# Kernel tuning notes

Hardware: AMD Instinct MI355X
Metric: run time of the kernel (lower is better)

Reference implementation:

```python
import jax, jax.numpy as jnp
import numpy as np

B, S, D = 2, 2048, 1024
H, HD = 16, 64
FF = 4096
LOCAL_W, RAND_P = 256, 0.2
EPS = 1e-5
NEG = -9e15


def _linear_params(key, din, dout):
    kw, kb = jax.random.split(key)
    bound = 1.0 / np.sqrt(din)
    W = jax.random.uniform(kw, (din, dout), jnp.float32, -bound, bound)
    b = jax.random.uniform(kb, (dout,), jnp.float32, -bound, bound)
    return W, b


def setup_inputs() -> dict:
    key = jax.random.key(0)
    ks = jax.random.split(key, 10)
    x = jax.random.normal(ks[0], (B, S, D), jnp.float32)
    # local + random mask, as in create_local_mask
    i = np.arange(S)[:, None]
    j = np.arange(S)[None, :]
    local = (np.abs(i - j) <= LOCAL_W // 2)
    rnd = np.asarray(jax.random.bernoulli(ks[1], RAND_P, (S, S)))
    mask = jnp.asarray(np.logical_or(local, rnd).astype(np.int32))
    Wq, bq = _linear_params(ks[2], D, D)
    Wk, bk = _linear_params(ks[3], D, D)
    Wv, bv = _linear_params(ks[4], D, D)
    Wo, bo = _linear_params(ks[5], D, D)
    W1, b1 = _linear_params(ks[6], D, FF)
    W2, b2 = _linear_params(ks[7], FF, D)
    g1 = jnp.ones((D,), jnp.float32); be1 = jnp.zeros((D,), jnp.float32)
    g2 = jnp.ones((D,), jnp.float32); be2 = jnp.zeros((D,), jnp.float32)
    return dict(x=x, mask=mask, Wq=Wq, bq=bq, Wk=Wk, bk=bk, Wv=Wv, bv=bv,
                Wo=Wo, bo=bo, W1=W1, b1=b1, W2=W2, b2=b2,
                g1=g1, be1=be1, g2=g2, be2=be2)


def _layernorm(x, g, b):
    mu = jnp.mean(x, axis=-1, keepdims=True)
    var = jnp.mean(jnp.square(x - mu), axis=-1, keepdims=True)
    return (x - mu) * jax.lax.rsqrt(var + EPS) * g + b


def reference(x, mask, Wq, bq, Wk, bk, Wv, bv, Wo, bo, W1, b1, W2, b2, g1, be1, g2, be2):
    scale = jnp.float32(np.sqrt(HD))  # sqrt(head_dim), requires_grad=False
    q = x @ Wq + bq
    k = x @ Wk + bk
    v = x @ Wv + bv
    # faithful to original: view(B, heads, S, head_dim) WITHOUT transpose
    q = q.reshape(B, H, S, HD)
    k = k.reshape(B, H, S, HD)
    v = v.reshape(B, H, S, HD)
    scores = jnp.einsum('bhsd,bhtd->bhst', q / scale, k)  # [B,H,S,S]
    scores = jnp.where(mask == 0, jnp.float32(NEG), scores)
    probs = jax.nn.softmax(scores, axis=-1)
    av = jnp.einsum('bhst,bhtd->bhsd', probs, v)
    # faithful reshape back: view(B, S, head_dim*heads)
    attn_out = av.reshape(B, S, H * HD) @ Wo + bo
    x = _layernorm(x + attn_out, g1, be1)
    ffn = jax.nn.gelu(x @ W1 + b1, approximate=False) @ W2 + b2
    x = _layernorm(x + ffn, g2, be2)
    return x
```

## Files before the change

kernel.cpp:

```cpp
#include <hip/hip_runtime.h>
#include <cstdint>
#include <cstddef>

namespace {

constexpr int kS  = 2048;
constexpr int kD  = 1024;
constexpr int kHD = 64;
constexpr int kTOK = 4096;

typedef float f32x4 __attribute__((ext_vector_type(4)));
typedef __bf16 bf16x8 __attribute__((ext_vector_type(8)));
typedef unsigned short u16x8 __attribute__((ext_vector_type(8)));

__device__ __forceinline__ unsigned short f2b(float f){
  unsigned int u = __builtin_bit_cast(unsigned int, f);
  u += 0x7fffu + ((u >> 16) & 1u);
  return (unsigned short)(u >> 16);
}

__device__ __forceinline__ float b2f(unsigned short u){
  return __builtin_bit_cast(float, (unsigned)u << 16);
}

__device__ __forceinline__ bf16x8 ldfrag(const unsigned short* p){
  return __builtin_bit_cast(bf16x8, *(const u16x8*)p);
}

__device__ __forceinline__ float fexp2(float x){
#if __has_builtin(__builtin_amdgcn_exp2f)
  return __builtin_amdgcn_exp2f(x);
#else
  return exp2f(x);
#endif
}

__device__ __forceinline__ void gl_lds16(const void* g, void* l){
  __builtin_amdgcn_global_load_lds(
      (__attribute__((address_space(1))) void*)(void*)g,
      (__attribute__((address_space(3))) void*)l, 16, 0, 0);
}

__device__ __forceinline__ bf16x8 ld_swz(const unsigned short* tile, int row, int slot){
  return ldfrag(tile + row * 64 + (((slot ^ row) & 7) << 3));
}

__device__ __forceinline__ void stageKt(const unsigned short* Kg, unsigned short* lds,
                                        int wave, int lane, int t0){
  #pragma unroll
  for (int i = 0; i < 2; ++i){
    const int lin = i * 4096 + wave * 1024 + lane * 16;
    const int r = lin >> 7;
    const int sl = (lin >> 4) & 7;
    const int sabs = t0 + r;
    gl_lds16(Kg + (size_t)(sabs >> 4) * 3072 + (sabs & 15) * 64 + (((sl ^ r) & 7) << 3),
             (char*)lds + i * 4096 + wave * 1024);
  }
}

__device__ __forceinline__ void stageVt(const unsigned short* Vh, unsigned short* lds,
                                        int wave, int lane, int t0){
  #pragma unroll
  for (int i = 0; i < 2; ++i){
    const int lin = i * 4096 + wave * 1024 + lane * 16;
    const int r = lin >> 7;
    const int sl = (lin >> 4) & 7;
    gl_lds16(Vh + (size_t)r * kS + t0 + (((sl ^ r) & 7) << 3),
             (char*)lds + i * 4096 + wave * 1024);
  }
}

__global__ __launch_bounds__(256) void cvt_bf16_kern(const float* __restrict__ X,
                                                     unsigned short* __restrict__ Y){
  int i = blockIdx.x * 256 + threadIdx.x;
  float4 v = ((const float4*)X)[i];
  ((ushort4*)Y)[i] = make_ushort4(f2b(v.x), f2b(v.y), f2b(v.z), f2b(v.w));
}

__global__ __launch_bounds__(256) void maskbits_kern(const int* __restrict__ mask,
                                                     unsigned long long* __restrict__ mb){
  const int gw   = (blockIdx.x * 256 + threadIdx.x) >> 6;
  const int lane = threadIdx.x & 63;
  const int row  = gw >> 5, word = gw & 31;
  const int key  = ((lane >> 2) & 3) * 16 + ((lane >> 4) & 3) * 4 + (lane & 3);
  const int m = mask[(size_t)row * kS + word * 64 + key];
  const unsigned long long b = __ballot(m != 0);
  if (lane == 0) mb[(size_t)row * 32 + word] = b;
}

__global__ __launch_bounds__(256) void catbias_kern(const float* __restrict__ a,
                                                    const float* __restrict__ b,
                                                    const float* __restrict__ c,
                                                    float* __restrict__ o){
  int i = blockIdx.x * 256 + threadIdx.x;
  float v = (i < 1024) ? a[i] : ((i < 2048) ? b[i - 1024] : c[i - 2048]);
  o[i] = v;
}

__global__ __launch_bounds__(256) void wtrans_kern(const float* __restrict__ W,
                                                   unsigned short* __restrict__ Wt,
                                                   int K, int N){
  __shared__ float t[32][33];
  int n0 = blockIdx.x * 32, k0 = blockIdx.y * 32;
  int tx = threadIdx.x & 31, ty = threadIdx.x >> 5;
  #pragma unroll
  for (int i = 0; i < 32; i += 8)
    t[ty + i][tx] = W[(size_t)(k0 + ty + i) * N + n0 + tx];
  __syncthreads();
  #pragma unroll
  for (int i = 0; i < 32; i += 8)
    Wt[(size_t)(n0 + ty + i) * K + k0 + tx] = f2b(t[tx][ty + i]);
}

__global__ __launch_bounds__(256) void vtrans_kern(const unsigned short* __restrict__ QKV,
                                                   unsigned short* __restrict__ Vt){
  __shared__ unsigned short t[64][65];
  int bh = blockIdx.y, s0 = blockIdx.x * 64;
  const int rowbase = (bh >> 4) * 2048 + (bh & 15) * 128;
  const unsigned short* Vg = QKV + (size_t)rowbase * 3072 + 2048;
  unsigned short* Vth = Vt + (size_t)bh * kHD * kS;
  int tx = threadIdx.x & 63, ty = threadIdx.x >> 6;
  #pragma unroll
  for (int i = 0; i < 64; i += 4){
    const int s = s0 + ty + i;
    t[ty + i][tx] = Vg[(size_t)(s >> 4) * 3072 + (s & 15) * 64 + tx];
  }
  __syncthreads();
  #pragma unroll
  for (int i = 0; i < 64; i += 4)
    Vth[(size_t)(ty + i) * kS + s0 + tx] = t[tx][ty + i];
}

template <int ACT_GELU, int SPLITK, int SCLQ>
__global__ __launch_bounds__(512, 2) void gemm256_kern(const unsigned short* __restrict__ A,
                                                       const unsigned short* __restrict__ Bt,
                                                       const float* __restrict__ bias,
                                                       unsigned short* __restrict__ C,
                                                       int M, int N, int K){
  __shared__ unsigned short As[2][2][128 * 64];
  __shared__ unsigned short Bs[2][2][128 * 64];
  int bid = blockIdx.y * gridDim.x + blockIdx.x;
  const int nwg = gridDim.x * gridDim.y;
  bid = (bid & 7) * (nwg >> 3) + (bid >> 3);
  const int bx = bid % gridDim.x, by = bid / gridDim.x;
  const int m0 = by << 8, n0 = bx << 8;
  const int tid  = threadIdx.x;
  const int wave = tid >> 6, lane = tid & 63;
  const int wr = wave >> 2, wc = wave & 3;
  const int lr = lane & 15, lk = lane >> 4;
  const int kz   = K / SPLITK;
  const int kbeg = (SPLITK > 1) ? blockIdx.z * kz : 0;
  const int NT   = kz >> 6;
  const int srow = tid >> 3;
  const int scol = ((tid & 7) ^ (srow & 7)) << 3;
  const unsigned short* Ag = A  + (size_t)(m0 + srow) * K + kbeg + scol;
  const unsigned short* Bg = Bt + (size_t)(n0 + srow) * K + kbeg + scol;
  const int dst = tid * 8;
  const int sk0 = ((    lk) ^ (lr & 7)) << 3;
  const int sk1 = ((4 + lk) ^ (lr & 7)) << 3;
  const int aro = lr * 64;
  const int bro = ((wc & 1) * 64 + lr) * 64;
  const int bh_ = wc >> 1;

  f32x4 acc[8][4] = {};
  bf16x8 aR[4][2], bR[2][2][2];

  auto stA = [&](int b, int h, int kt){
    const unsigned short* s = Ag + (size_t)(h * 128) * K + kt * 64;
    gl_lds16(s,                  &As[b][h][dst]);
    gl_lds16(s + (size_t)64 * K, &As[b][h][4096 + dst]);
  };
  auto stB = [&](int b, int h, int kt){
    const unsigned short* s = Bg + (size_t)(h * 128) * K + kt * 64;
    gl_lds16(s,                  &Bs[b][h][dst]);
    gl_lds16(s + (size_t)64 * K, &Bs[b][h][4096 + dst]);
  };

#define LOAD_A(b, MH) { \
  _Pragma("unroll") for (int mp = 0; mp < 4; ++mp){ \
    aR[mp][0] = ldfrag(&As[b][wr][aro + ((MH) * 64 + mp * 16) * 64 + sk0]); \
    aR[mp][1] = ldfrag(&As[b][wr][aro + ((MH) * 64 + mp * 16) * 64 + sk1]); } }
#define LOAD_B(b, NH) { \
  _Pragma("unroll") for (int np = 0; np < 2; ++np){ \
    bR[NH][np][0] = ldfrag(&Bs[b][bh_][bro + ((NH) * 32 + np * 16) * 64 + sk0]); \
    bR[NH][np][1] = ldfrag(&Bs[b][bh_][bro + ((NH) * 32 + np * 16) * 64 + sk1]); } }
#define QMFMA(MH, NH) { \
  _Pragma("unroll") for (int kk = 0; kk < 2; ++kk) \
  _Pragma("unroll") for (int mp = 0; mp < 4; ++mp) \
  _Pragma("unroll") for (int np = 0; np < 2; ++np) \
    acc[(MH)*4+mp][(NH)*2+np] = __builtin_amdgcn_mfma_f32_16x16x32_bf16( \
        aR[mp][kk], bR[NH][np][kk], acc[(MH)*4+mp][(NH)*2+np], 0, 0, 0); }
#define PHASE_TAIL(QM) \
  asm volatile("s_barrier" ::: "memory"); \
  asm volatile("s_waitcnt lgkmcnt(0)" ::: "memory"); \
  __builtin_amdgcn_sched_barrier(0); \
  __builtin_amdgcn_s_setprio(1); \
  QM; \
  __builtin_amdgcn_s_setprio(0); \
  __builtin_amdgcn_sched_barrier(0); \
  asm volatile("s_barrier" ::: "memory");

  stA(0, 0, 0); stB(0, 0, 0); stB(0, 1, 0); stA(0, 1, 0);
  asm volatile("s_waitcnt vmcnt(4)" ::: "memory");
  asm volatile("s_barrier" ::: "memory");

  for (int t = 0; t < NT; ++t){
    const int b = t & 1, bn = b ^ 1;
    const bool pf = (t + 1 < NT);
    LOAD_A(b, 0); LOAD_B(b, 0);
    if (pf){ stA(bn, 0, t + 1); asm volatile("s_waitcnt vmcnt(4)" ::: "memory"); }
    else   {                    asm volatile("s_waitcnt vmcnt(2)" ::: "memory"); }
    PHASE_TAIL(QMFMA(0, 0));
    LOAD_B(b, 1);
    if (pf){ stB(bn, 0, t + 1); asm volatile("s_waitcnt vmcnt(4)" ::: "memory"); }
    else   {                    asm volatile("s_waitcnt vmcnt(0)" ::: "memory"); }
    PHASE_TAIL(QMFMA(0, 1));
    LOAD_A(b, 1);
    if (pf){ stB(bn, 1, t + 1); }
    PHASE_TAIL(QMFMA(1, 0));
    if (pf){ stA(bn, 1, t + 1); asm volatile("s_waitcnt vmcnt(4)" ::: "memory"); }
    PHASE_TAIL(QMFMA(1, 1));
  }
#undef LOAD_A
#undef LOAD_B
#undef QMFMA
#undef PHASE_TAIL

  unsigned short* Cb = C + (SPLITK > 1 ? (size_t)blockIdx.z * M * N : 0);
  float bvv[4], csc[4];
  #pragma unroll
  for (int n = 0; n < 4; ++n){
    const int col = n0 + wc * 64 + n * 16 + lr;
    bvv[n] = (SPLITK == 1) ? bias[col] : 0.0f;
    csc[n] = (SCLQ && col < 1024) ? 0.18033688011112042f : 1.0f;
  }
  #pragma unroll
  for (int m = 0; m < 8; ++m){
    #pragma unroll
    for (int j = 0; j < 4; ++j){
      const int row = m0 + wr * 128 + m * 16 + lk * 4 + j;
      unsigned short* crow = Cb + (size_t)row * N + n0 + wc * 64 + lr;
      #pragma unroll
      for (int n = 0; n < 4; ++n){
        float v = acc[m][n][j] + bvv[n];
        if (ACT_GELU) v = 0.5f * v * (1.0f + erff(v * 0.70710678118654752f));
        if (SCLQ) v *= csc[n];
        crow[n * 16] = f2b(v);
      }
    }
  }
}

__global__ __launch_bounds__(256) void attn_kern(const unsigned short* __restrict__ QKV,
                                                 const unsigned short* __restrict__ Vt,
                                                 const unsigned long long* __restrict__ mbits,
                                                 unsigned short* __restrict__ O){
  __shared__ unsigned short Ks[2][64 * 64];
  __shared__ unsigned short Vs[2][64 * 64];
  __shared__ unsigned short Ps[4][16 * 64];
  const int tid = threadIdx.x;
  const int wave = tid >> 6, lane = tid & 63;
  const int lr = lane & 15, lk = lane >> 4;
  int bid = blockIdx.y * gridDim.x + blockIdx.x;
  bid = (bid & 7) * 128 + (bid >> 3);
  const int qblk = bid & 31, bh = bid >> 5;
  const int rowbase = (bh >> 4) * 2048 + (bh & 15) * 128;
  const unsigned short* Qg = QKV + (size_t)rowbase * 3072;
  const unsigned short* Kg = Qg + 1024;
  const unsigned short* Vh = Vt + (size_t)bh * kHD * kS;
  const int qbase = qblk * 64 + wave * 16;

  bf16x8 qf[2];
  { const int qr = qbase + lr;
    const unsigned short* qp = Qg + (size_t)(qr >> 4) * 3072 + (qr & 15) * 64 + lk * 8;
    qf[0] = ldfrag(qp); qf[1] = ldfrag(qp + 32); }

  f32x4 accO[4] = {};
  float lsum = 0.f;
  unsigned short* Pw = Ps[wave];
  char* Pwb = (char*)Pw + lr * 128 + ((lk & 1) << 3);
  const int lr7 = lr & 7;

  const unsigned long long* mrp = mbits + (size_t)(qbase + lr) * 32;
  unsigned long long mb = mrp[0];

  stageKt(Kg, Ks[0], wave, lane, 0);
  stageVt(Vh, Vs[0], wave, lane, 0);
  __syncthreads();

  int cur = 0;
  for (int t = 0; t < kS / 64; ++t){
    unsigned long long mbn = 0;
    if (t < kS / 64 - 1){
      stageKt(Kg, Ks[cur ^ 1], wave, lane, (t + 1) * 64);
      stageVt(Vh, Vs[cur ^ 1], wave, lane, (t + 1) * 64);
      mbn = mrp[t + 1];
    }
    f32x4 sa[4] = {};
    #pragma unroll
    for (int kk = 0; kk < 2; ++kk)
      #pragma unroll
      for (int n = 0; n < 4; ++n){
        bf16x8 kf = ld_swz(Ks[cur], n * 16 + lr, kk * 4 + lk);
        sa[n] = __builtin_amdgcn_mfma_f32_16x16x32_bf16(kf, qf[kk], sa[n], 0, 0, 0);
      }
    const unsigned wb = (unsigned)(mb >> (lk * 16));
    float s = 0.f;
    #pragma unroll
    for (int n = 0; n < 4; ++n){
      float p0, p1, p2, p3;
      {
        float v0 = fexp2(sa[n][0]), v1 = fexp2(sa[n][1]);
        float v2 = fexp2(sa[n][2]), v3 = fexp2(sa[n][3]);
        const int s0 = ((int)(wb << (31 - (n * 4 + 0)))) >> 31;
        const int s1 = ((int)(wb << (31 - (n * 4 + 1)))) >> 31;
        const int s2 = ((int)(wb << (31 - (n * 4 + 2)))) >> 31;
        const int s3 = ((int)(wb << (31 - (n * 4 + 3)))) >> 31;
        p0 = __builtin_bit_cast(float, __builtin_bit_cast(int, v0) & s0);
        p1 = __builtin_bit_cast(float, __builtin_bit_cast(int, v1) & s1);
        p2 = __builtin_bit_cast(float, __builtin_bit_cast(int, v2) & s2);
        p3 = __builtin_bit_cast(float, __builtin_bit_cast(int, v3) & s3);
      }
      s += (p0 + p1) + (p2 + p3);
      unsigned r0, r1;
      asm("v_cvt_pk_bf16_f32 %0, %1, %2" : "=v"(r0) : "v"(p0), "v"(p1));
      asm("v_cvt_pk_bf16_f32 %0, %1, %2" : "=v"(r1) : "v"(p2), "v"(p3));
      *(uint2*)(Pwb + (((2 * n + (lk >> 1)) ^ lr7) << 4)) = make_uint2(r0, r1);
    }
    s += __shfl_xor(s, 16);
    s += __shfl_xor(s, 32);
    lsum += s;
    #pragma unroll
    for (int kk = 0; kk < 2; ++kk){
      bf16x8 pf = ld_swz(Pw, lr, kk * 4 + lk);
      #pragma unroll
      for (int dd = 0; dd < 4; ++dd){
        bf16x8 vfr = ld_swz(Vs[cur], dd * 16 + lr, kk * 4 + lk);
        accO[dd] = __builtin_amdgcn_mfma_f32_16x16x32_bf16(pf, vfr, accO[dd], 0, 0, 0);
      }
    }
    mb = mbn;
    __syncthreads();
    cur ^= 1;
  }
  const size_t hoff = (size_t)bh * kS * kHD;
  #pragma unroll
  for (int j = 0; j < 4; ++j){
    const float inv = 1.0f / __shfl(lsum, lk * 4 + j);
    const int row = qbase + lk * 4 + j;
    #pragma unroll
    for (int dd = 0; dd < 4; ++dd)
      O[hoff + (size_t)row * 64 + dd * 16 + lr] = f2b(accO[dd][j] * inv);
  }
}

template <int NP, int PBF16, int OUT_B>
__global__ __launch_bounds__(256) void add_ln_kern(const float* __restrict__ X,
                                                   const void* __restrict__ P,
                                                   const float* __restrict__ bias,
                                                   const float* __restrict__ g,
                                                   const float* __restrict__ be,
                                                   float* __restrict__ Yf,
                                                   unsigned short* __restrict__ Yb){
  const int row = blockIdx.x;
  const int tid = threadIdx.x;
  const size_t pstride = (size_t)kTOK * kD;
  const int idx = row * 256 + tid;
  float r0 = 0.f, r1 = 0.f, r2 = 0.f, r3 = 0.f;
  #pragma unroll
  for (int z = 0; z < NP; ++z){
    if (PBF16){
      ushort4 u = ((const ushort4*)P)[z * (pstride / 4) + idx];
      r0 += b2f(u.x); r1 += b2f(u.y); r2 += b2f(u.z); r3 += b2f(u.w);
    } else {
      float4 p = ((const float4*)P)[z * (pstride / 4) + idx];
      r0 += p.x; r1 += p.y; r2 += p.z; r3 += p.w;
    }
  }
  const float4 bb = ((const float4*)bias)[tid];
  const float4 xv = ((const float4*)X)[idx];
  const float a0 = xv.x + r0 + bb.x, a1 = xv.y + r1 + bb.y;
  const float a2 = xv.z + r2 + bb.z, a3 = xv.w + r3 + bb.w;
  float s = a0 + a1 + a2 + a3;
  float q = a0*a0 + a1*a1 + a2*a2 + a3*a3;
  #pragma unroll
  for (int d = 1; d < 64; d <<= 1){ s += __shfl_xor(s, d); q += __shfl_xor(q, d); }
  __shared__ float red[8];
  const int wave = tid >> 6, lane = tid & 63;
  if (lane == 0){ red[wave] = s; red[4 + wave] = q; }
  __syncthreads();
  s = red[0] + red[1] + red[2] + red[3];
  q = red[4] + red[5] + red[6] + red[7];
  const float mu   = s * (1.0f / kD);
  const float var  = q * (1.0f / kD) - mu * mu;
  const float rstd = rsqrtf(var + 1e-5f);
  const float4 gv = ((const float4*)g)[tid];
  const float4 bv = ((const float4*)be)[tid];
  const float y0 = (a0 - mu) * rstd * gv.x + bv.x;
  const float y1 = (a1 - mu) * rstd * gv.y + bv.y;
  const float y2 = (a2 - mu) * rstd * gv.z + bv.z;
  const float y3 = (a3 - mu) * rstd * gv.w + bv.w;
  ((float4*)Yf)[idx] = make_float4(y0, y1, y2, y3);
  if (OUT_B)
    ((ushort4*)Yb)[idx] = make_ushort4(f2b(y0), f2b(y1), f2b(y2), f2b(y3));
}

}

extern "C" void kernel_launch(void* const* d_in, const int* in_sizes, int n_in,
                              void* d_out, int out_size, void* d_ws, size_t ws_size,
                              hipStream_t stream){
  (void)in_sizes; (void)n_in; (void)out_size;
  const float* x   = (const float*)d_in[0];
  const int*   mask= (const int*)d_in[1];
  const float* Wq  = (const float*)d_in[2];  const float* bq  = (const float*)d_in[3];
  const float* Wk  = (const float*)d_in[4];  const float* bk  = (const float*)d_in[5];
  const float* Wv  = (const float*)d_in[6];  const float* bv  = (const float*)d_in[7];
  const float* Wo  = (const float*)d_in[8];  const float* bo  = (const float*)d_in[9];
  const float* W1  = (const float*)d_in[10]; const float* b1  = (const float*)d_in[11];
  const float* W2  = (const float*)d_in[12]; const float* b2  = (const float*)d_in[13];
  const float* g1  = (const float*)d_in[14]; const float* be1 = (const float*)d_in[15];
  const float* g2  = (const float*)d_in[16]; const float* be2 = (const float*)d_in[17];

  char* ws = (char*)d_ws;
  const size_t MB = 1024 * 1024;
  if (ws_size < 96 * MB) return;

  unsigned short* W2T   = (unsigned short*)(ws + 0 * MB);
  unsigned short* W1T   = (unsigned short*)(ws + 8 * MB);
  unsigned short* WqkvT = (unsigned short*)(ws + 16 * MB);
  unsigned short* WoT   = (unsigned short*)(ws + 22 * MB);
  unsigned short* xb    = (unsigned short*)(ws + 24 * MB);
  unsigned short* qkv   = (unsigned short*)(ws + 32 * MB);
  unsigned short* vt    = (unsigned short*)(ws + 56 * MB);
  unsigned short* av    = (unsigned short*)(ws + 64 * MB);
  unsigned long long* mbits = (unsigned long long*)(ws + 72 * MB);
  float* bqkv           = (float*)(ws + 80 * MB);
  unsigned short* woP   = (unsigned short*)(ws + 32 * MB);
  float* y32            = (float*)(ws + 72 * MB);
  unsigned short* yb    = (unsigned short*)(ws + 88 * MB);
  unsigned short* hb    = (unsigned short*)(ws + 40 * MB);
  unsigned short* w2p   = (unsigned short*)(ws + 8 * MB);

  dim3 blk(256), gblk(512);
  wtrans_kern<<<dim3(32, 32),  blk, 0, stream>>>(Wq, WqkvT,                   1024, 1024);
  wtrans_kern<<<dim3(32, 32),  blk, 0, stream>>>(Wk, WqkvT + 1024 * 1024,     1024, 1024);
  wtrans_kern<<<dim3(32, 32),  blk, 0, stream>>>(Wv, WqkvT + 2 * 1024 * 1024, 1024, 1024);
  wtrans_kern<<<dim3(32, 32),  blk, 0, stream>>>(Wo, WoT, 1024, 1024);
  wtrans_kern<<<dim3(128, 32), blk, 0, stream>>>(W1, W1T, 1024, 4096);
  wtrans_kern<<<dim3(32, 128), blk, 0, stream>>>(W2, W2T, 4096, 1024);
  cvt_bf16_kern<<<dim3(kTOK * kD / 1024), blk, 0, stream>>>(x, xb);
  maskbits_kern<<<dim3(kS * 32 / 4), blk, 0, stream>>>(mask, mbits);
  catbias_kern<<<dim3(12), blk, 0, stream>>>(bq, bk, bv, bqkv);

  gemm256_kern<0,1,1><<<dim3(12, 16), gblk, 0, stream>>>(xb, WqkvT, bqkv, qkv, 4096, 3072, 1024);

  vtrans_kern<<<dim3(32, 32), blk, 0, stream>>>(qkv, vt);
  attn_kern<<<dim3(32, 32), blk, 0, stream>>>(qkv, vt, mbits, av);

  gemm256_kern<0,4,0><<<dim3(4, 16, 4), gblk, 0, stream>>>(av, WoT, bo, woP, 4096, 1024, 1024);
  add_ln_kern<4,1,1><<<dim3(4096), blk, 0, stream>>>(x, woP, bo, g1, be1, y32, yb);

  gemm256_kern<1,1,0><<<dim3(16, 16), gblk, 0, stream>>>(yb, W1T, b1, hb, 4096, 4096, 1024);
  gemm256_kern<0,4,0><<<dim3(4, 16, 4), gblk, 0, stream>>>(hb, W2T, b2, w2p, 4096, 1024, 4096);
  add_ln_kern<4,1,0><<<dim3(4096), blk, 0, stream>>>(y32, w2p, b2, g2, be2, (float*)d_out, nullptr);
}
```

Measured before the change: 268.4 us.

## Merge prep launches, widen attention blocks to 128 queries, use fast erf

The six weight-transpose launches become one kernel, and the bf16 convert, mask-bit and bias-concat launches become another, which cuts launch overhead. The attention kernel now runs 512 threads covering 128 queries per block, so each staged K/V tile is shared by twice as many query rows and global K/V traffic drops, at the cost of more waves waiting on each barrier. GELU now uses an Abramowitz-Stegun polynomial approximation of erf with a hardware reciprocal instead of erff, which costs less arithmetic but loses some accuracy.

```diff
diff --git a/kernel.cpp b/kernel.cpp
--- a/kernel.cpp
+++ b/kernel.cpp
@@ -35,6 +35,19 @@
 #endif
 }
 
+__device__ __forceinline__ float fast_erf(float x){
+  const float ax = fabsf(x);
+#if __has_builtin(__builtin_amdgcn_rcpf)
+  const float t = __builtin_amdgcn_rcpf(1.0f + 0.3275911f * ax);
+#else
+  const float t = 1.0f / (1.0f + 0.3275911f * ax);
+#endif
+  const float y = t * (0.254829592f + t * (-0.284496736f + t * (1.421413741f +
+                  t * (-1.453152027f + t * 1.061405429f))));
+  const float e = fexp2(-ax * ax * 1.4426950408889634f);
+  return copysignf(1.0f - y * e, x);
+}
+
 __device__ __forceinline__ void gl_lds16(const void* g, void* l){
   __builtin_amdgcn_global_load_lds(
       (__attribute__((address_space(1))) void*)(void*)g,
@@ -45,64 +58,70 @@
   return ldfrag(tile + row * 64 + (((slot ^ row) & 7) << 3));
 }
 
-__device__ __forceinline__ void stageKt(const unsigned short* Kg, unsigned short* lds,
-                                        int wave, int lane, int t0){
-  #pragma unroll
-  for (int i = 0; i < 2; ++i){
-    const int lin = i * 4096 + wave * 1024 + lane * 16;
-    const int r = lin >> 7;
-    const int sl = (lin >> 4) & 7;
-    const int sabs = t0 + r;
-    gl_lds16(Kg + (size_t)(sabs >> 4) * 3072 + (sabs & 15) * 64 + (((sl ^ r) & 7) << 3),
-             (char*)lds + i * 4096 + wave * 1024);
-  }
-}
-
-__device__ __forceinline__ void stageVt(const unsigned short* Vh, unsigned short* lds,
-                                        int wave, int lane, int t0){
-  #pragma unroll
-  for (int i = 0; i < 2; ++i){
-    const int lin = i * 4096 + wave * 1024 + lane * 16;
-    const int r = lin >> 7;
-    const int sl = (lin >> 4) & 7;
-    gl_lds16(Vh + (size_t)r * kS + t0 + (((sl ^ r) & 7) << 3),
-             (char*)lds + i * 4096 + wave * 1024);
-  }
-}
-
-__global__ __launch_bounds__(256) void cvt_bf16_kern(const float* __restrict__ X,
-                                                     unsigned short* __restrict__ Y){
-  int i = blockIdx.x * 256 + threadIdx.x;
-  float4 v = ((const float4*)X)[i];
-  ((ushort4*)Y)[i] = make_ushort4(f2b(v.x), f2b(v.y), f2b(v.z), f2b(v.w));
-}
-
-__global__ __launch_bounds__(256) void maskbits_kern(const int* __restrict__ mask,
-                                                     unsigned long long* __restrict__ mb){
-  const int gw   = (blockIdx.x * 256 + threadIdx.x) >> 6;
-  const int lane = threadIdx.x & 63;
-  const int row  = gw >> 5, word = gw & 31;
-  const int key  = ((lane >> 2) & 3) * 16 + ((lane >> 4) & 3) * 4 + (lane & 3);
-  const int m = mask[(size_t)row * kS + word * 64 + key];
-  const unsigned long long b = __ballot(m != 0);
-  if (lane == 0) mb[(size_t)row * 32 + word] = b;
-}
-
-__global__ __launch_bounds__(256) void catbias_kern(const float* __restrict__ a,
-                                                    const float* __restrict__ b,
-                                                    const float* __restrict__ c,
-                                                    float* __restrict__ o){
-  int i = blockIdx.x * 256 + threadIdx.x;
-  float v = (i < 1024) ? a[i] : ((i < 2048) ? b[i - 1024] : c[i - 2048]);
-  o[i] = v;
-}
-
-__global__ __launch_bounds__(256) void wtrans_kern(const float* __restrict__ W,
-                                                   unsigned short* __restrict__ Wt,
-                                                   int K, int N){
+__device__ __forceinline__ void stageK8(const unsigned short* Kg, unsigned short* lds,
+                                        int tid, int t0){
+  const int r = tid >> 3, sl = tid & 7;
+  const int sabs = t0 + r;
+  gl_lds16(Kg + (size_t)(sabs >> 4) * 3072 + (sabs & 15) * 64 + (((sl ^ r) & 7) << 3),
+           (char*)lds + tid * 16);
+}
+
+__device__ __forceinline__ void stageV8(const unsigned short* Vh, unsigned short* lds,
+                                        int tid, int t0){
+  const int r = tid >> 3, sl = tid & 7;
+  gl_lds16(Vh + (size_t)r * kS + t0 + (((sl ^ r) & 7) << 3),
+           (char*)lds + tid * 16);
+}
+
+__global__ __launch_bounds__(256) void prep_misc_kern(const float* __restrict__ x,
+                                                      unsigned short* __restrict__ xb,
+                                                      const int* __restrict__ mask,
+                                                      unsigned long long* __restrict__ mb,
+                                                      const float* __restrict__ bq,
+                                                      const float* __restrict__ bk,
+                                                      const float* __restrict__ bv,
+                                                      float* __restrict__ bqkv){
+  const int b = blockIdx.x;
+  if (b < 4096){
+    const int i = b * 256 + threadIdx.x;
+    float4 v = ((const float4*)x)[i];
+    ((ushort4*)xb)[i] = make_ushort4(f2b(v.x), f2b(v.y), f2b(v.z), f2b(v.w));
+  } else if (b < 20480){
+    const int gw   = ((b - 4096) * 256 + threadIdx.x) >> 6;
+    const int lane = threadIdx.x & 63;
+    const int row  = gw >> 5, word = gw & 31;
+    const int key  = ((lane >> 2) & 3) * 16 + ((lane >> 4) & 3) * 4 + (lane & 3);
+    const int m = mask[(size_t)row * kS + word * 64 + key];
+    const unsigned long long bl = __ballot(m != 0);
+    if (lane == 0) mb[(size_t)row * 32 + word] = bl;
+  } else {
+    const int i = (b - 20480) * 256 + threadIdx.x;
+    float v = (i < 1024) ? bq[i] : ((i < 2048) ? bk[i - 1024] : bv[i - 2048]);
+    bqkv[i] = v;
+  }
+}
+
+__global__ __launch_bounds__(256) void wtrans_all_kern(const float* __restrict__ Wq,
+                                                       const float* __restrict__ Wk,
+                                                       const float* __restrict__ Wv,
+                                                       const float* __restrict__ Wo,
+                                                       const float* __restrict__ W1,
+                                                       const float* __restrict__ W2,
+                                                       unsigned short* __restrict__ WqkvT,
+                                                       unsigned short* __restrict__ WoT,
+                                                       unsigned short* __restrict__ W1T,
+                                                       unsigned short* __restrict__ W2T){
+  const int b = blockIdx.x;
+  const float* W; unsigned short* Wt; int K, N, nx, lb;
+  if      (b < 1024){ W = Wq; Wt = WqkvT;                 K = 1024; N = 1024; nx = 32;  lb = b; }
+  else if (b < 2048){ W = Wk; Wt = WqkvT + 1024 * 1024;   K = 1024; N = 1024; nx = 32;  lb = b - 1024; }
+  else if (b < 3072){ W = Wv; Wt = WqkvT + 2048 * 1024;   K = 1024; N = 1024; nx = 32;  lb = b - 2048; }
+  else if (b < 4096){ W = Wo; Wt = WoT;                   K = 1024; N = 1024; nx = 32;  lb = b - 3072; }
+  else if (b < 8192){ W = W1; Wt = W1T;                   K = 1024; N = 4096; nx = 128; lb = b - 4096; }
+  else              { W = W2; Wt = W2T;                   K = 4096; N = 1024; nx = 32;  lb = b - 8192; }
   __shared__ float t[32][33];
-  int n0 = blockIdx.x * 32, k0 = blockIdx.y * 32;
-  int tx = threadIdx.x & 31, ty = threadIdx.x >> 5;
+  const int n0 = (lb % nx) * 32, k0 = (lb / nx) * 32;
+  const int tx = threadIdx.x & 31, ty = threadIdx.x >> 5;
   #pragma unroll
   for (int i = 0; i < 32; i += 8)
     t[ty + i][tx] = W[(size_t)(k0 + ty + i) * N + n0 + tx];
@@ -243,7 +262,7 @@
       #pragma unroll
       for (int n = 0; n < 4; ++n){
         float v = acc[m][n][j] + bvv[n];
-        if (ACT_GELU) v = 0.5f * v * (1.0f + erff(v * 0.70710678118654752f));
+        if (ACT_GELU) v = 0.5f * v * (1.0f + fast_erf(v * 0.70710678118654752f));
         if (SCLQ) v *= csc[n];
         crow[n * 16] = f2b(v);
       }
@@ -251,24 +270,24 @@
   }
 }
 
-__global__ __launch_bounds__(256) void attn_kern(const unsigned short* __restrict__ QKV,
+__global__ __launch_bounds__(512) void attn_kern(const unsigned short* __restrict__ QKV,
                                                  const unsigned short* __restrict__ Vt,
                                                  const unsigned long long* __restrict__ mbits,
                                                  unsigned short* __restrict__ O){
   __shared__ unsigned short Ks[2][64 * 64];
   __shared__ unsigned short Vs[2][64 * 64];
-  __shared__ unsigned short Ps[4][16 * 64];
+  __shared__ unsigned short Ps[8][16 * 64];
   const int tid = threadIdx.x;
   const int wave = tid >> 6, lane = tid & 63;
   const int lr = lane & 15, lk = lane >> 4;
   int bid = blockIdx.y * gridDim.x + blockIdx.x;
-  bid = (bid & 7) * 128 + (bid >> 3);
-  const int qblk = bid & 31, bh = bid >> 5;
+  bid = (bid & 7) * 64 + (bid >> 3);
+  const int qblk = bid & 15, bh = bid >> 4;
   const int rowbase = (bh >> 4) * 2048 + (bh & 15) * 128;
   const unsigned short* Qg = QKV + (size_t)rowbase * 3072;
   const unsigned short* Kg = Qg + 1024;
   const unsigned short* Vh = Vt + (size_t)bh * kHD * kS;
-  const int qbase = qblk * 64 + wave * 16;
+  const int qbase = qblk * 128 + wave * 16;
 
   bf16x8 qf[2];
   { const int qr = qbase + lr;
@@ -284,16 +303,16 @@
   const unsigned long long* mrp = mbits + (size_t)(qbase + lr) * 32;
   unsigned long long mb = mrp[0];
 
-  stageKt(Kg, Ks[0], wave, lane, 0);
-  stageVt(Vh, Vs[0], wave, lane, 0);
+  stageK8(Kg, Ks[0], tid, 0);
+  stageV8(Vh, Vs[0], tid, 0);
   __syncthreads();
 
   int cur = 0;
   for (int t = 0; t < kS / 64; ++t){
     unsigned long long mbn = 0;
     if (t < kS / 64 - 1){
-      stageKt(Kg, Ks[cur ^ 1], wave, lane, (t + 1) * 64);
-      stageVt(Vh, Vs[cur ^ 1], wave, lane, (t + 1) * 64);
+      stageK8(Kg, Ks[cur ^ 1], tid, (t + 1) * 64);
+      stageV8(Vh, Vs[cur ^ 1], tid, (t + 1) * 64);
       mbn = mrp[t + 1];
     }
     f32x4 sa[4] = {};
@@ -443,20 +462,14 @@
   unsigned short* w2p   = (unsigned short*)(ws + 8 * MB);
 
   dim3 blk(256), gblk(512);
-  wtrans_kern<<<dim3(32, 32),  blk, 0, stream>>>(Wq, WqkvT,                   1024, 1024);
-  wtrans_kern<<<dim3(32, 32),  blk, 0, stream>>>(Wk, WqkvT + 1024 * 1024,     1024, 1024);
-  wtrans_kern<<<dim3(32, 32),  blk, 0, stream>>>(Wv, WqkvT + 2 * 1024 * 1024, 1024, 1024);
-  wtrans_kern<<<dim3(32, 32),  blk, 0, stream>>>(Wo, WoT, 1024, 1024);
-  wtrans_kern<<<dim3(128, 32), blk, 0, stream>>>(W1, W1T, 1024, 4096);
-  wtrans_kern<<<dim3(32, 128), blk, 0, stream>>>(W2, W2T, 4096, 1024);
-  cvt_bf16_kern<<<dim3(kTOK * kD / 1024), blk, 0, stream>>>(x, xb);
-  maskbits_kern<<<dim3(kS * 32 / 4), blk, 0, stream>>>(mask, mbits);
-  catbias_kern<<<dim3(12), blk, 0, stream>>>(bq, bk, bv, bqkv);
+  wtrans_all_kern<<<dim3(12288), blk, 0, stream>>>(Wq, Wk, Wv, Wo, W1, W2,
+                                                   WqkvT, WoT, W1T, W2T);
+  prep_misc_kern<<<dim3(20492), blk, 0, stream>>>(x, xb, mask, mbits, bq, bk, bv, bqkv);
 
   gemm256_kern<0,1,1><<<dim3(12, 16), gblk, 0, stream>>>(xb, WqkvT, bqkv, qkv, 4096, 3072, 1024);
 
   vtrans_kern<<<dim3(32, 32), blk, 0, stream>>>(qkv, vt);
-  attn_kern<<<dim3(32, 32), blk, 0, stream>>>(qkv, vt, mbits, av);
+  attn_kern<<<dim3(16, 32), gblk, 0, stream>>>(qkv, vt, mbits, av);
 
   gemm256_kern<0,4,0><<<dim3(4, 16, 4), gblk, 0, stream>>>(av, WoT, bo, woP, 4096, 1024, 1024);
   add_ln_kern<4,1,1><<<dim3(4096), blk, 0, stream>>>(x, woP, bo, g1, be1, y32, yb);
```

New measurement: 241.5 us. -10.0%, faster.
